# Optimization experiments

Hardware: AMD Instinct MI355X
Metric: run time of the kernel (lower is better)

Reference implementation:

```python
import math
import jax, jax.numpy as jnp
import numpy as np

B, H, W, DIM, HEADS, K = 4, 56, 56, 512, 16, 7


def setup_inputs() -> dict:
    key = jax.random.key(0)
    ks = jax.random.split(key, 8)
    s = 1.0 / math.sqrt(DIM)
    return {
        "hidden_states": jax.random.normal(ks[0], (B, H, W, DIM), jnp.float32),
        "Wq": jax.random.normal(ks[1], (DIM, DIM), jnp.float32) * s,
        "bq": jnp.zeros((DIM,), jnp.float32),
        "Wk": jax.random.normal(ks[2], (DIM, DIM), jnp.float32) * s,
        "bk": jnp.zeros((DIM,), jnp.float32),
        "Wv": jax.random.normal(ks[3], (DIM, DIM), jnp.float32) * s,
        "bv": jnp.zeros((DIM,), jnp.float32),
        "rpb": jax.random.normal(ks[4], (HEADS, 2 * K - 1, 2 * K - 1), jnp.float32) * 0.02,
    }


def reference(hidden_states, Wq, bq, Wk, bk, Wv, bv, rpb):
    b, h_sz, w_sz, dim = hidden_states.shape
    heads = rpb.shape[0]
    k = (rpb.shape[1] + 1) // 2  # rpb is [heads, 2k-1, 2k-1]
    d = dim // heads

    def split_heads(x):
        # [B,H,W,dim] -> [B,heads,H,W,d]  (matches transpose_for_scores permute(0,3,1,2,4))
        return x.reshape(b, h_sz, w_sz, heads, d).transpose(0, 3, 1, 2, 4)

    q = split_heads(hidden_states @ Wq.T + bq) / jnp.sqrt(jnp.asarray(d, hidden_states.dtype))
    key = split_heads(hidden_states @ Wk.T + bk)
    val = split_heads(hidden_states @ Wv.T + bv)

    half = k // 2
    ii = jnp.arange(h_sz)
    ni = jnp.clip(ii - half, 0, h_sz - k)  # neighborhood row start per query row (NATTEN edge clamping)
    jj = jnp.arange(w_sz)
    nj = jnp.clip(jj - half, 0, w_sz - k)

    # natten2dqkrpb: windowed QK with relative position bias (loop over k*k kernel offsets,
    # which mirrors the fused kernel's inner loop and avoids a [B,h,H,W,k,k,d] gather blowup)
    scores = []
    for ki in range(k):
        ridx = ni + ki                      # [H] key row index per query row
        bi = ridx - ii + (k - 1)            # [H] relative bias row index
        key_r = key[:, :, ridx]             # [B,h,H,W,d]
        rpb_r = rpb[:, bi]                  # [h,H,2k-1]
        for kj in range(k):
            cidx = nj + kj                  # [W]
            bj = cidx - jj + (k - 1)        # [W]
            key_rc = key_r[:, :, :, cidx]   # [B,h,H,W,d]
            s = jnp.einsum('bhijd,bhijd->bhij', q, key_rc)
            scores.append(s + rpb_r[:, :, bj][None])  # add bias [1,h,H,W]
    scores = jnp.stack(scores, axis=-1)     # [B,h,H,W,k*k]

    probs = jax.nn.softmax(scores, axis=-1)  # dropout p=0.0 -> identity

    # natten2dav: windowed AV
    ctx = jnp.zeros_like(q)                 # [B,h,H,W,d]
    idx = 0
    for ki in range(k):
        v_r = val[:, :, ni + ki]
        for kj in range(k):
            ctx = ctx + probs[..., idx, None] * v_r[:, :, :, nj + kj]
            idx += 1

    # permute(0,2,3,1,4) then merge heads
    return ctx.transpose(0, 2, 3, 1, 4).reshape(b, h_sz, w_sz, dim)
```

## Files before the change

kernel.cpp:

```cpp
#include <hip/hip_runtime.h>
#include <stdint.h>

typedef unsigned short u16;
typedef __bf16 bf16x8 __attribute__((ext_vector_type(8)));
typedef float f32x4 __attribute__((ext_vector_type(4)));

#define M_PIX 12544
#define DIMC  512
#define NQKV  1536

static __device__ __forceinline__ u16 f2bf(float f) {
  union { float f; uint32_t u; } x; x.f = f;
  uint32_t r = x.u + 0x7FFFu + ((x.u >> 16) & 1u);
  return (u16)(r >> 16);
}

__global__ void cast_all(const float* __restrict__ x, const float* __restrict__ Wq,
                         const float* __restrict__ Wk, const float* __restrict__ Wv,
                         u16* __restrict__ Xb, u16* __restrict__ Wc) {
  int idx = (blockIdx.x * 256 + threadIdx.x) * 4;
  const int NX = M_PIX * DIMC;
  const float* src;
  u16* dst;
  if (idx < NX) {
    src = x + idx; dst = Xb + idx;
  } else {
    int wi = idx - NX;
    if (wi >= NQKV * DIMC) return;
    int r = wi >> 9;
    int c = wi & 511;
    src = (r < 512)  ? (Wq + (size_t)r * 512 + c)
        : (r < 1024) ? (Wk + (size_t)(r - 512) * 512 + c)
                     : (Wv + (size_t)(r - 1024) * 512 + c);
    dst = Wc + wi;
  }
  float4 f = *(const float4*)src;
  uint32_t p0 = (uint32_t)f2bf(f.x) | ((uint32_t)f2bf(f.y) << 16);
  uint32_t p1 = (uint32_t)f2bf(f.z) | ((uint32_t)f2bf(f.w) << 16);
  *(uint2*)dst = make_uint2(p0, p1);
}

__global__ __launch_bounds__(256, 4) void gemm_qkv(
    const u16* __restrict__ A, const u16* __restrict__ Bm,
    const float* __restrict__ bq, const float* __restrict__ bk,
    const float* __restrict__ bv, u16* __restrict__ qkv) {
  __shared__ u16 sA[2][128 * 32];
  __shared__ u16 sB[2][128 * 32];
  const int t = threadIdx.x;
  const int lane = t & 63;
  const int w = t >> 6;
  const int bid = blockIdx.x;
  const int g = (bid & 7) * 147 + (bid >> 3);
  const int tile_m = (g / 12) * 128;
  const int tile_n = (g % 12) * 128;
  const int wm = (w & 1) * 64;
  const int wn = (w >> 1) * 64;
  const int quad = lane >> 4;
  const int l16 = lane & 15;

  f32x4 acc[4][4];
#pragma unroll
  for (int a = 0; a < 4; ++a)
#pragma unroll
    for (int bb = 0; bb < 4; ++bb) acc[a][bb] = (f32x4){0.f, 0.f, 0.f, 0.f};

  const int c0 = t, c1 = t + 256;
  const int r0 = c0 >> 2, ko0 = (c0 & 3) * 8;
  const int r1 = c1 >> 2, ko1 = (c1 & 3) * 8;
  const u16* gA0 = A + (size_t)(tile_m + r0) * DIMC + ko0;
  const u16* gA1 = A + (size_t)(tile_m + r1) * DIMC + ko1;
  const u16* gB0 = Bm + (size_t)(tile_n + r0) * DIMC + ko0;
  const u16* gB1 = Bm + (size_t)(tile_n + r1) * DIMC + ko1;
  const int ldsoff = (t & ~63) * 8;

  for (int k0 = 0; k0 < DIMC; k0 += 64) {
#pragma unroll
    for (int h = 0; h < 2; ++h) {
      __builtin_amdgcn_global_load_lds(
          (const __attribute__((address_space(1))) void*)(gA0 + k0 + h * 32),
          (__attribute__((address_space(3))) void*)(sA[h] + 0 * 2048 + ldsoff), 16, 0, 0);
      __builtin_amdgcn_global_load_lds(
          (const __attribute__((address_space(1))) void*)(gA1 + k0 + h * 32),
          (__attribute__((address_space(3))) void*)(sA[h] + 1 * 2048 + ldsoff), 16, 0, 0);
      __builtin_amdgcn_global_load_lds(
          (const __attribute__((address_space(1))) void*)(gB0 + k0 + h * 32),
          (__attribute__((address_space(3))) void*)(sB[h] + 0 * 2048 + ldsoff), 16, 0, 0);
      __builtin_amdgcn_global_load_lds(
          (const __attribute__((address_space(1))) void*)(gB1 + k0 + h * 32),
          (__attribute__((address_space(3))) void*)(sB[h] + 1 * 2048 + ldsoff), 16, 0, 0);
    }
    __syncthreads();

#pragma unroll
    for (int h = 0; h < 2; ++h) {
      bf16x8 af[4], bfr[4];
#pragma unroll
      for (int mt = 0; mt < 4; ++mt)
        af[mt] = *(const bf16x8*)(sA[h] + (wm + mt * 16 + l16) * 32 + quad * 8);
#pragma unroll
      for (int nt = 0; nt < 4; ++nt)
        bfr[nt] = *(const bf16x8*)(sB[h] + (wn + nt * 16 + l16) * 32 + quad * 8);
#pragma unroll
      for (int mt = 0; mt < 4; ++mt)
#pragma unroll
        for (int nt = 0; nt < 4; ++nt)
          acc[mt][nt] = __builtin_amdgcn_mfma_f32_16x16x32_bf16(bfr[nt], af[mt], acc[mt][nt], 0, 0, 0);
    }
    __syncthreads();
  }

  const float qscale = 0.17677669529663687f;
#pragma unroll
  for (int mt = 0; mt < 4; ++mt) {
    const int m = tile_m + wm + mt * 16 + l16;
#pragma unroll
    for (int nt = 0; nt < 4; ++nt) {
      const int n0 = tile_n + wn + nt * 16 + quad * 4;
      const int mat = n0 >> 9;
      const int cc = n0 & 511;
      const float* bias = (mat == 0) ? bq : (mat == 1) ? bk : bv;
      const float4 bv4 = *(const float4*)(bias + cc);
      const float scl = (mat == 0) ? qscale : 1.0f;
      u16 h0 = f2bf((acc[mt][nt][0] + bv4.x) * scl);
      u16 h1 = f2bf((acc[mt][nt][1] + bv4.y) * scl);
      u16 h2 = f2bf((acc[mt][nt][2] + bv4.z) * scl);
      u16 h3 = f2bf((acc[mt][nt][3] + bv4.w) * scl);
      uint2 pk = make_uint2((uint32_t)h0 | ((uint32_t)h1 << 16),
                            (uint32_t)h2 | ((uint32_t)h3 << 16));
      *(uint2*)(qkv + (size_t)mat * M_PIX * DIMC + (size_t)m * DIMC + cc) = pk;
    }
  }
}

__global__ __launch_bounds__(512, 4) void natten_k(const u16* __restrict__ qkv,
                                                   const float* __restrict__ rpb,
                                                   float* __restrict__ out) {
  __shared__ u16 uShared[21504];
  __shared__ u16 sVt[32 * 296];
  __shared__ float sRpb[256];
  __shared__ uint32_t sTbl[320];
  u16* sK = uShared;
  u16* sP = uShared;

  const int tid = threadIdx.x;
  const int lane = tid & 63;
  const int w = tid >> 6;
  const int l16 = lane & 15;
  const int quad = lane >> 4;

  const int bid = blockIdx.x;
  const int xcd = bid & 7;
  const int idx = bid >> 3;
  const int head = idx / 14;
  const int gl = idx - head * 14;
  const int g = xcd * 14 + gl;
  const int jg = g & 3;
  const int gi = g >> 2;
  const int b = gi / 7;
  const int ig = gi - b * 7;
  const int i0 = ig * 8, j0 = jg * 14;
  int c0 = j0 - 3; c0 = c0 < 0 ? 0 : (c0 > 36 ? 36 : c0);
  int nib = i0 - 3; nib = nib < 0 ? 0 : (nib > 49 ? 49 : nib);

  const int iw = i0 + w;
  int niw = iw - 3; niw = niw < 0 ? 0 : (niw > 49 ? 49 : niw);
  const int rowoff = niw - nib;
  const int par = rowoff & 1;
  const int woff2 = rowoff * 20 - par * 4;
  const int wconst = niw - iw + 6;

  const int qv = l16 < 14 ? l16 : 13;
  const int jq = j0 + qv;
  int njq = jq - 3; njq = njq < 0 ? 0 : (njq > 49 ? 49 : njq);
  const uint32_t offq = (uint32_t)(njq - c0);
  const int Cq = wconst * 13 + (c0 - jq + 6);

  const u16* Kpl = qkv + (size_t)M_PIX * DIMC;

  union { uint4 u; bf16x8 v; } qu;
  qu.u = make_uint4(0, 0, 0, 0);
  if (l16 < 14) {
    size_t qpx = (size_t)((b * 56 + iw) * 56 + j0 + l16);
    qu.u = *(const uint4*)(qkv + qpx * DIMC + head * 32 + quad * 8);
  }
  const bf16x8 qf = qu.v;

  for (int it = 0; it < 3; ++it) {
    int task = it * 512 + tid;
    if (task < 1184) {
      int cand = task >> 2, dg = task & 3;
      int r = (cand * 205) >> 12;
      int c = cand - r * 20;
      int rimg = nib + r;
      uint4 kk = make_uint4(0, 0, 0, 0);
      if (rimg < 56) {
        size_t px = (size_t)((b * 56 + rimg) * 56 + c0 + c);
        kk = *(const uint4*)(Kpl + px * DIMC + head * 32 + dg * 8);
      }
      *(uint4*)((char*)sK + cand * 80 + dg * 16) = kk;
    }
  }
  {
    const int cp = tid;
    if (cp < 148) {
      int cand0 = cp * 2;
      int r = (cand0 * 205) >> 12;
      int c = cand0 - r * 20;
      int rimg = nib + r;
      const bool ok = (rimg < 56);
      size_t px = (size_t)((b * 56 + rimg) * 56 + c0 + c);
      const u16* vsrc = Kpl + (size_t)M_PIX * DIMC + px * DIMC + head * 32;
      u16* vt = sVt + cand0;
#pragma unroll
      for (int dg = 0; dg < 4; ++dg) {
        uint4 va = ok ? *(const uint4*)(vsrc + dg * 8) : make_uint4(0, 0, 0, 0);
        uint4 vb = ok ? *(const uint4*)(vsrc + DIMC + dg * 8) : make_uint4(0, 0, 0, 0);
        int d0 = dg * 8;
        *(uint32_t*)(vt + (d0 + 0) * 296) = __builtin_amdgcn_perm(vb.x, va.x, 0x05040100u);
        *(uint32_t*)(vt + (d0 + 1) * 296) = __builtin_amdgcn_perm(vb.x, va.x, 0x07060302u);
        *(uint32_t*)(vt + (d0 + 2) * 296) = __builtin_amdgcn_perm(vb.y, va.y, 0x05040100u);
        *(uint32_t*)(vt + (d0 + 3) * 296) = __builtin_amdgcn_perm(vb.y, va.y, 0x07060302u);
        *(uint32_t*)(vt + (d0 + 4) * 296) = __builtin_amdgcn_perm(vb.z, va.z, 0x05040100u);
        *(uint32_t*)(vt + (d0 + 5) * 296) = __builtin_amdgcn_perm(vb.z, va.z, 0x07060302u);
        *(uint32_t*)(vt + (d0 + 6) * 296) = __builtin_amdgcn_perm(vb.w, va.w, 0x05040100u);
        *(uint32_t*)(vt + (d0 + 7) * 296) = __builtin_amdgcn_perm(vb.w, va.w, 0x07060302u);
      }
    }
  }
  if (tid < 256) sRpb[tid] = (tid < 169) ? rpb[head * 169 + tid] : 0.f;
  if (tid < 320) {
    int pp = tid >= 160 ? 1 : 0;
    int s = tid - pp * 160;
    int t0 = s - pp * 4;
    uint32_t e = 255u;
    if (t0 >= 0 && t0 < 140) {
      int r = (t0 * 205) >> 12;
      int c = t0 - r * 20;
      e = (uint32_t)c | ((uint32_t)(r * 13 + c) << 8);
    }
    sTbl[tid] = e;
  }
  __syncthreads();

  u16* sPw = sP + w * 2688;
  f32x4 S[10];
#pragma unroll
  for (int ch = 0; ch < 10; ++ch) {
    bf16x8 kf = *(const bf16x8*)((char*)sK + (woff2 + ch * 16 + l16) * 80 + quad * 16);
    S[ch] = __builtin_amdgcn_mfma_f32_16x16x32_bf16(kf, qf, (f32x4){0.f, 0.f, 0.f, 0.f}, 0, 0, 0);
  }

  __syncthreads();

  const float LOG2E = 1.4426950408889634f;
  float l = 0.f;
  const uint32_t* tb = sTbl + par * 160;
#pragma unroll
  for (int ch = 0; ch < 10; ++ch) {
    uint4 te = *(const uint4*)(tb + ch * 16 + quad * 4);
    float pv[4];
    uint32_t es[4] = {te.x, te.y, te.z, te.w};
#pragma unroll
    for (int rg = 0; rg < 4; ++rg) {
      uint32_t e = es[rg];
      uint32_t ce = e & 255u;
      bool valid = (ce - offq) < 7u;
      int ridx = (int)((e >> 8) & 255u) + Cq;
      float rb = sRpb[ridx];
      float p = exp2f((S[ch][rg] + rb) * LOG2E);
      p = valid ? p : 0.f;
      pv[rg] = p;
      l += p;
    }
    uint32_t plo, phi;
    asm("v_cvt_pk_bf16_f32 %0, %1, %2" : "=v"(plo) : "v"(pv[0]), "v"(pv[1]));
    asm("v_cvt_pk_bf16_f32 %0, %1, %2" : "=v"(phi) : "v"(pv[2]), "v"(pv[3]));
    *(uint2*)((char*)sPw + l16 * 336 + ch * 32 + quad * 8) = make_uint2(plo, phi);
  }
  l += __shfl_xor(l, 16);
  l += __shfl_xor(l, 32);

  __syncthreads();

  f32x4 O0 = (f32x4){0.f, 0.f, 0.f, 0.f};
  f32x4 O1 = (f32x4){0.f, 0.f, 0.f, 0.f};
#pragma unroll
  for (int c32 = 0; c32 < 5; ++c32) {
    bf16x8 pf = *(const bf16x8*)((char*)sPw + l16 * 336 + c32 * 64 + quad * 16);
    bf16x8 v0 = *(const bf16x8*)((char*)sVt + (0 + l16) * 592 + woff2 * 2 + c32 * 64 + quad * 16);
    bf16x8 v1 = *(const bf16x8*)((char*)sVt + (16 + l16) * 592 + woff2 * 2 + c32 * 64 + quad * 16);
    O0 = __builtin_amdgcn_mfma_f32_16x16x32_bf16(v0, pf, O0, 0, 0, 0);
    O1 = __builtin_amdgcn_mfma_f32_16x16x32_bf16(v1, pf, O1, 0, 0, 0);
  }

  if (l16 < 14) {
    const float inv = 1.0f / l;
    float* op = out + ((size_t)((b * 56 + iw) * 56 + j0 + l16)) * DIMC + head * 32;
    *(float4*)(op + quad * 4) =
        make_float4(O0[0] * inv, O0[1] * inv, O0[2] * inv, O0[3] * inv);
    *(float4*)(op + 16 + quad * 4) =
        make_float4(O1[0] * inv, O1[1] * inv, O1[2] * inv, O1[3] * inv);
  }
}

extern "C" void kernel_launch(void* const* d_in, const int* in_sizes, int n_in,
                              void* d_out, int out_size, void* d_ws, size_t ws_size,
                              hipStream_t stream) {
  const float* x   = (const float*)d_in[0];
  const float* Wq  = (const float*)d_in[1];
  const float* bq  = (const float*)d_in[2];
  const float* Wk  = (const float*)d_in[3];
  const float* bk  = (const float*)d_in[4];
  const float* Wv  = (const float*)d_in[5];
  const float* bv  = (const float*)d_in[6];
  const float* rpb = (const float*)d_in[7];
  float* out = (float*)d_out;

  u16* Xb  = (u16*)d_ws;
  u16* Wc  = Xb + (size_t)M_PIX * DIMC;
  u16* qkv = Wc + (size_t)NQKV * DIMC;

  const int ncast = (M_PIX * DIMC + NQKV * DIMC) / 4;
  cast_all<<<(ncast + 255) / 256, 256, 0, stream>>>(x, Wq, Wk, Wv, Xb, Wc);
  gemm_qkv<<<1176, 256, 0, stream>>>(Xb, Wc, bq, bk, bv, qkv);
  natten_k<<<1792, 512, 0, stream>>>(qkv, rpb, out);
}
```

Measured before the change: 158.1 us.

## Load K fragments directly into registers and split V transpose across more threads

K tiles no longer pass through shared memory. Each lane loads its bf16x8 K fragments straight from global memory into registers, which removes the K staging stores and one block barrier, and sP gets its own LDS buffer instead of aliasing sK. The V transpose-load now uses 296 threads, each handling half the head dims, so more of the load runs in parallel. In exchange, K rows shared by overlapping windows are fetched redundantly from global/L2, and the out-of-image row guard (rimg<56) is dropped for K, which may read beyond the image for edge candidates.

After: 153.2 us. 3.1% less time.

```diff
diff --git a/kernel.cpp b/kernel.cpp
--- a/kernel.cpp
+++ b/kernel.cpp
@@ -135,12 +135,10 @@
 __global__ __launch_bounds__(512, 4) void natten_k(const u16* __restrict__ qkv,
                                                    const float* __restrict__ rpb,
                                                    float* __restrict__ out) {
-  __shared__ u16 uShared[21504];
+  __shared__ u16 sP[8 * 2688];
   __shared__ u16 sVt[32 * 296];
   __shared__ float sRpb[256];
   __shared__ uint32_t sTbl[320];
-  u16* sK = uShared;
-  u16* sP = uShared;
 
   const int tid = threadIdx.x;
   const int lane = tid & 63;
@@ -185,46 +183,29 @@
   }
   const bf16x8 qf = qu.v;
 
-  for (int it = 0; it < 3; ++it) {
-    int task = it * 512 + tid;
-    if (task < 1184) {
-      int cand = task >> 2, dg = task & 3;
-      int r = (cand * 205) >> 12;
-      int c = cand - r * 20;
-      int rimg = nib + r;
-      uint4 kk = make_uint4(0, 0, 0, 0);
-      if (rimg < 56) {
-        size_t px = (size_t)((b * 56 + rimg) * 56 + c0 + c);
-        kk = *(const uint4*)(Kpl + px * DIMC + head * 32 + dg * 8);
-      }
-      *(uint4*)((char*)sK + cand * 80 + dg * 16) = kk;
-    }
-  }
-  {
-    const int cp = tid;
-    if (cp < 148) {
-      int cand0 = cp * 2;
-      int r = (cand0 * 205) >> 12;
-      int c = cand0 - r * 20;
-      int rimg = nib + r;
-      const bool ok = (rimg < 56);
-      size_t px = (size_t)((b * 56 + rimg) * 56 + c0 + c);
-      const u16* vsrc = Kpl + (size_t)M_PIX * DIMC + px * DIMC + head * 32;
-      u16* vt = sVt + cand0;
-#pragma unroll
-      for (int dg = 0; dg < 4; ++dg) {
-        uint4 va = ok ? *(const uint4*)(vsrc + dg * 8) : make_uint4(0, 0, 0, 0);
-        uint4 vb = ok ? *(const uint4*)(vsrc + DIMC + dg * 8) : make_uint4(0, 0, 0, 0);
-        int d0 = dg * 8;
-        *(uint32_t*)(vt + (d0 + 0) * 296) = __builtin_amdgcn_perm(vb.x, va.x, 0x05040100u);
-        *(uint32_t*)(vt + (d0 + 1) * 296) = __builtin_amdgcn_perm(vb.x, va.x, 0x07060302u);
-        *(uint32_t*)(vt + (d0 + 2) * 296) = __builtin_amdgcn_perm(vb.y, va.y, 0x05040100u);
-        *(uint32_t*)(vt + (d0 + 3) * 296) = __builtin_amdgcn_perm(vb.y, va.y, 0x07060302u);
-        *(uint32_t*)(vt + (d0 + 4) * 296) = __builtin_amdgcn_perm(vb.z, va.z, 0x05040100u);
-        *(uint32_t*)(vt + (d0 + 5) * 296) = __builtin_amdgcn_perm(vb.z, va.z, 0x07060302u);
-        *(uint32_t*)(vt + (d0 + 6) * 296) = __builtin_amdgcn_perm(vb.w, va.w, 0x05040100u);
-        *(uint32_t*)(vt + (d0 + 7) * 296) = __builtin_amdgcn_perm(vb.w, va.w, 0x07060302u);
-      }
+  if (tid < 296) {
+    const int pair = tid >> 1, half = tid & 1;
+    const int cand0 = pair * 2;
+    int r = (cand0 * 205) >> 12;
+    int c = cand0 - r * 20;
+    int rimg = nib + r;
+    const bool ok = (rimg < 56);
+    size_t px = (size_t)((b * 56 + rimg) * 56 + c0 + c);
+    const u16* vsrc = Kpl + (size_t)M_PIX * DIMC + px * DIMC + head * 32 + half * 16;
+    u16* vt = sVt + cand0;
+#pragma unroll
+    for (int dgh = 0; dgh < 2; ++dgh) {
+      uint4 va = ok ? *(const uint4*)(vsrc + dgh * 8) : make_uint4(0, 0, 0, 0);
+      uint4 vb = ok ? *(const uint4*)(vsrc + DIMC + dgh * 8) : make_uint4(0, 0, 0, 0);
+      int d0 = (half * 2 + dgh) * 8;
+      *(uint32_t*)(vt + (d0 + 0) * 296) = __builtin_amdgcn_perm(vb.x, va.x, 0x05040100u);
+      *(uint32_t*)(vt + (d0 + 1) * 296) = __builtin_amdgcn_perm(vb.x, va.x, 0x07060302u);
+      *(uint32_t*)(vt + (d0 + 2) * 296) = __builtin_amdgcn_perm(vb.y, va.y, 0x05040100u);
+      *(uint32_t*)(vt + (d0 + 3) * 296) = __builtin_amdgcn_perm(vb.y, va.y, 0x07060302u);
+      *(uint32_t*)(vt + (d0 + 4) * 296) = __builtin_amdgcn_perm(vb.z, va.z, 0x05040100u);
+      *(uint32_t*)(vt + (d0 + 5) * 296) = __builtin_amdgcn_perm(vb.z, va.z, 0x07060302u);
+      *(uint32_t*)(vt + (d0 + 6) * 296) = __builtin_amdgcn_perm(vb.w, va.w, 0x05040100u);
+      *(uint32_t*)(vt + (d0 + 7) * 296) = __builtin_amdgcn_perm(vb.w, va.w, 0x07060302u);
     }
   }
   if (tid < 256) sRpb[tid] = (tid < 169) ? rpb[head * 169 + tid] : 0.f;
@@ -240,17 +221,26 @@
     }
     sTbl[tid] = e;
   }
+
+  const int pxbase = (b * 56 + nib) * 56 + c0;
+  const u16* kbase = Kpl + (size_t)head * 32 + quad * 8;
+  bf16x8 kreg[10];
+#pragma unroll
+  for (int ch = 0; ch < 10; ++ch) {
+    int cand = woff2 + ch * 16 + l16;
+    int r = (cand * 205) >> 12;
+    int c = cand - r * 20;
+    int px = pxbase + r * 56 + c;
+    kreg[ch] = *(const bf16x8*)(kbase + (size_t)px * DIMC);
+  }
+
   __syncthreads();
 
   u16* sPw = sP + w * 2688;
   f32x4 S[10];
 #pragma unroll
-  for (int ch = 0; ch < 10; ++ch) {
-    bf16x8 kf = *(const bf16x8*)((char*)sK + (woff2 + ch * 16 + l16) * 80 + quad * 16);
-    S[ch] = __builtin_amdgcn_mfma_f32_16x16x32_bf16(kf, qf, (f32x4){0.f, 0.f, 0.f, 0.f}, 0, 0, 0);
-  }
-
-  __syncthreads();
+  for (int ch = 0; ch < 10; ++ch)
+    S[ch] = __builtin_amdgcn_mfma_f32_16x16x32_bf16(kreg[ch], qf, (f32x4){0.f, 0.f, 0.f, 0.f}, 0, 0, 0);
 
   const float LOG2E = 1.4426950408889634f;
   float l = 0.f;
```
